# Kernel tuning notes

Measured on AMD Instinct MI355X. Metric: run time of the kernel, lower is better.

## Reference

```python
import jax, jax.numpy as jnp
import numpy as np

DIM = 1024
HEADS = 16
DIM_HEAD = 64


def setup_inputs() -> dict:
    key = jax.random.key(0)
    ks = jax.random.split(key, 6)
    b, n = 2, 2048
    x = jax.random.normal(ks[0], (b, n, DIM), dtype=jnp.float32)
    gamma = jnp.ones((DIM,), dtype=jnp.float32)
    w_qkv = jax.random.normal(ks[1], (DIM, 3 * HEADS * DIM_HEAD), dtype=jnp.float32) * (DIM ** -0.5)
    w_gates = jax.random.normal(ks[2], (DIM, HEADS), dtype=jnp.float32) * (DIM ** -0.5)
    b_gates = jnp.zeros((HEADS,), dtype=jnp.float32)
    w_out = jax.random.normal(ks[3], (HEADS * DIM_HEAD, DIM), dtype=jnp.float32) * ((HEADS * DIM_HEAD) ** -0.5)
    freqs = jax.random.uniform(ks[4], (DIM_HEAD // 2,), dtype=jnp.float32)
    return {"x": x, "gamma": gamma, "w_qkv": w_qkv, "w_gates": w_gates,
            "b_gates": b_gates, "w_out": w_out, "freqs": freqs}


def _rotate_half(t):
    # interleaved pairs: (x1, x2) -> (-x2, x1)
    tp = t.reshape(t.shape[:-1] + (t.shape[-1] // 2, 2))
    x1, x2 = tp[..., 0], tp[..., 1]
    return jnp.stack((-x2, x1), axis=-1).reshape(t.shape)


def reference(x, gamma, w_qkv, w_gates, b_gates, w_out, freqs):
    b, n, d = x.shape
    # RMSNorm variant: divide by L2 norm, scale by gamma * sqrt(dim)
    xn = x / jnp.linalg.norm(x, axis=-1, keepdims=True)
    xn = xn * gamma * (d ** 0.5)
    # QKV projection: (b, n, 3*H*D) -> q,k,v each (b, h, n, dh)
    qkv = xn @ w_qkv
    qkv = qkv.reshape(b, n, 3, HEADS, DIM_HEAD).transpose(2, 0, 3, 1, 4)
    q, k, v = qkv[0], qkv[1], qkv[2]
    # Inline RoPE (interleaved): freqs (n, dh)
    pos = jnp.arange(n, dtype=freqs.dtype)
    f = jnp.repeat(pos[:, None] * freqs[None, :], 2, axis=-1)  # (n, dh)
    cos_f, sin_f = jnp.cos(f), jnp.sin(f)
    q = q * cos_f + _rotate_half(q) * sin_f
    k = k * cos_f + _rotate_half(k) * sin_f
    # SDPA
    scale = DIM_HEAD ** -0.5
    scores = jnp.einsum('bhqd,bhkd->bhqk', q, k) * scale
    attn = jax.nn.softmax(scores, axis=-1)
    out = jnp.einsum('bhqk,bhkd->bhqd', attn, v)  # (b, h, n, dh)
    # per-head sigmoid gate from normalized input
    gates = xn @ w_gates + b_gates  # (b, n, h)
    out = out * jax.nn.sigmoid(gates.transpose(0, 2, 1))[..., None]
    # merge heads and output projection
    out = out.transpose(0, 2, 1, 3).reshape(b, n, HEADS * DIM_HEAD)
    return out @ w_out
```

## Files before the change

### kernel.cpp

```cpp
#include <hip/hip_runtime.h>

typedef __bf16 bf16_t;
typedef __bf16 bf16x8 __attribute__((ext_vector_type(8)));
typedef __bf16 bf16x4 __attribute__((ext_vector_type(4)));
typedef float f32x4 __attribute__((ext_vector_type(4)));

#define B_  2
#define N_  2048
#define D_  1024
#define H_  16
#define DH_ 64

#define QSCALE 0.18033688011112042f
#define NEGC  -11.541560327111707f

#if __has_builtin(__builtin_amdgcn_exp2f)
#define EXP2F(x) __builtin_amdgcn_exp2f(x)
#else
#define EXP2F(x) exp2f(x)
#endif

#define GLL16(g, l) __builtin_amdgcn_global_load_lds( \
    (const __attribute__((address_space(1))) void*)(g), \
    (__attribute__((address_space(3))) void*)(l), 16, 0, 0)

__device__ __forceinline__ int xcd_swizzle_id() {
  int id = blockIdx.y * gridDim.x + blockIdx.x;
  int cpx = (gridDim.x * gridDim.y) >> 3;
  return (id & 7) * cpx + (id >> 3);
}

__global__ __launch_bounds__(256) void k_trig(const float* __restrict__ freqs,
    float* __restrict__ tc, float* __restrict__ ts) {
  int idx = blockIdx.x * 256 + threadIdx.x;
  int n = idx >> 5, j = idx & 31;
  float f = (float)n * freqs[j];
  tc[idx] = cosf(f);
  ts[idx] = sinf(f);
}

__global__ __launch_bounds__(256) void k_rmsnorm_gates(const float* __restrict__ x,
    const float* __restrict__ gamma, const float* __restrict__ wg,
    const float* __restrict__ bg, bf16_t* __restrict__ xn, float* __restrict__ gsig) {
  int row = blockIdx.x;
  const float4* xr = (const float4*)(x + (size_t)row * D_);
  int tid = threadIdx.x;
  float4 v = xr[tid];
  float ss = v.x*v.x + v.y*v.y + v.z*v.z + v.w*v.w;
  #pragma unroll
  for (int off = 32; off > 0; off >>= 1) ss += __shfl_down(ss, off);
  __shared__ float red4[4];
  if ((tid & 63) == 0) red4[tid >> 6] = ss;
  __syncthreads();
  float scale = 32.0f * rsqrtf(red4[0] + red4[1] + red4[2] + red4[3]);
  float4 g = ((const float4*)gamma)[tid];
  bf16x4 o;
  o[0] = (bf16_t)(v.x * scale * g.x);
  o[1] = (bf16_t)(v.y * scale * g.y);
  o[2] = (bf16_t)(v.z * scale * g.z);
  o[3] = (bf16_t)(v.w * scale * g.w);
  *(bf16x4*)(xn + (size_t)row * D_ + tid * 4) = o;
  float xv[4] = {(float)o[0], (float)o[1], (float)o[2], (float)o[3]};
  float part[16];
  #pragma unroll
  for (int h = 0; h < 16; ++h) part[h] = 0.f;
  #pragma unroll
  for (int j = 0; j < 4; ++j) {
    const float4* wr = (const float4*)&wg[(size_t)(tid * 4 + j) * 16];
    #pragma unroll
    for (int q = 0; q < 4; ++q) {
      float4 w4 = wr[q];
      part[q * 4 + 0] += xv[j] * w4.x;
      part[q * 4 + 1] += xv[j] * w4.y;
      part[q * 4 + 2] += xv[j] * w4.z;
      part[q * 4 + 3] += xv[j] * w4.w;
    }
  }
  __shared__ float red[256][17];
  #pragma unroll
  for (int h = 0; h < 16; ++h) red[tid][h] = part[h];
  __syncthreads();
  int h = tid & 15, grp = tid >> 4;
  float s = 0.f;
  #pragma unroll
  for (int k = 0; k < 16; ++k) s += red[grp * 16 + k][h];
  __syncthreads();
  red[grp][h] = s;
  __syncthreads();
  if (tid < 16) {
    float acc = bg[tid];
    #pragma unroll
    for (int k = 0; k < 16; ++k) acc += red[k][tid];
    gsig[(size_t)row * 16 + tid] = 1.0f / (1.0f + __expf(-acc));
  }
}

__global__ __launch_bounds__(256) void k_transpose_cvt(const float* __restrict__ W,
    bf16_t* __restrict__ Wt, int R, int C) {
  __shared__ float tile[32][33];
  int c0 = blockIdx.x * 32, r0 = blockIdx.y * 32;
  int tx = threadIdx.x & 31, ty = threadIdx.x >> 5;
  #pragma unroll
  for (int i = 0; i < 4; ++i) {
    int r = ty + i * 8;
    tile[r][tx] = W[(size_t)(r0 + r) * C + c0 + tx];
  }
  __syncthreads();
  #pragma unroll
  for (int i = 0; i < 4; ++i) {
    int rr = ty + i * 8;
    Wt[(size_t)(c0 + rr) * R + r0 + tx] = (bf16_t)tile[tx][rr];
  }
}

__global__ __launch_bounds__(256) void k_gemm_qkv(const bf16_t* __restrict__ A,
    const bf16_t* __restrict__ Bt, const float* __restrict__ tc,
    const float* __restrict__ ts, bf16_t* __restrict__ Qb,
    bf16_t* __restrict__ Kb, bf16_t* __restrict__ Vb) {
  constexpr int BK = 32, K = 1024;
  constexpr int TP = 136;
  __shared__ __align__(16) bf16_t As[128 * BK];
  __shared__ __align__(16) bf16_t Bs[128 * BK];
  __shared__ __align__(16) bf16_t Tt[128 * TP];
  int tid = threadIdx.x, wave = tid >> 6, lane = tid & 63;
  int l16 = lane & 15, quad = lane >> 4;
  int id = blockIdx.y * 32 + blockIdx.x;
  int xcd = id & 7, local = id >> 3;
  int bxi = (xcd & 3) * 8 + (local & 7);
  int byi = (xcd >> 2) * 12 + (local >> 3);
  int bm = bxi * 128, bn = byi * 128;
  int wm = (wave >> 1) * 64, wn = (wave & 1) * 64;
  int srow = wave * 32 + (lane >> 2);
  int scol = (lane & 3) * 8;
  const bf16_t* gA0 = &A [(size_t)(bm + srow)      * K + scol];
  const bf16_t* gA1 = &A [(size_t)(bm + srow + 16) * K + scol];
  const bf16_t* gB0 = &Bt[(size_t)(bn + srow)      * K + scol];
  const bf16_t* gB1 = &Bt[(size_t)(bn + srow + 16) * K + scol];
  bf16_t* lA0 = &As[(wave * 32)      * BK];
  bf16_t* lA1 = &As[(wave * 32 + 16) * BK];
  bf16_t* lB0 = &Bs[(wave * 32)      * BK];
  bf16_t* lB1 = &Bs[(wave * 32 + 16) * BK];
  f32x4 acc[4][4] = {};
  for (int k0 = 0; k0 < K; k0 += BK) {
    GLL16(gA0 + k0, lA0);
    GLL16(gA1 + k0, lA1);
    GLL16(gB0 + k0, lB0);
    GLL16(gB1 + k0, lB1);
    __syncthreads();
    bf16x8 af[4], bfr[4];
    #pragma unroll
    for (int t = 0; t < 4; ++t) {
      af[t]  = *(const bf16x8*)&As[(wm + t * 16 + l16) * BK + quad * 8];
      bfr[t] = *(const bf16x8*)&Bs[(wn + t * 16 + l16) * BK + quad * 8];
    }
    #pragma unroll
    for (int mt = 0; mt < 4; ++mt)
      #pragma unroll
      for (int nt = 0; nt < 4; ++nt)
        acc[mt][nt] = __builtin_amdgcn_mfma_f32_16x16x32_bf16(af[mt], bfr[nt], acc[mt][nt], 0, 0, 0);
    __syncthreads();
  }
  if (byi < 16) {
    float qs = (byi < 8) ? QSCALE : 1.0f;
    bf16_t* dst = (byi < 8) ? Qb : Kb;
    #pragma unroll
    for (int mt = 0; mt < 4; ++mt)
      #pragma unroll
      for (int r = 0; r < 4; ++r) {
        int row_l = wm + mt * 16 + quad * 4 + r;
        int n = (bm + row_l) & 2047;
        const float* cr = tc + n * 32;
        const float* sr = ts + n * 32;
        #pragma unroll
        for (int nt = 0; nt < 4; ++nt) {
          int col_l = wn + nt * 16 + l16;
          int d = (bn + col_l) & 63, j = d >> 1;
          float val = acc[mt][nt][r];
          float p = __shfl_xor(val, 1);
          float c = cr[j], s = sr[j];
          float o = (d & 1) ? (val * c + p * s) : (val * c - p * s);
          Tt[row_l * TP + col_l] = (bf16_t)(o * qs);
        }
      }
    __syncthreads();
    #pragma unroll
    for (int it = 0; it < 8; ++it) {
      int idx = tid + 256 * it;
      int row_l = idx >> 4, ck = (idx & 15) * 8;
      bf16x8 v = *(const bf16x8*)&Tt[row_l * TP + ck];
      int grow = bm + row_l, b = grow >> 11, n = grow & 2047;
      int col = bn + ck, h = (col >> 6) & 15, d = col & 63;
      *(bf16x8*)&dst[((size_t)(b * H_ + h) * N_ + n) * DH_ + d] = v;
    }
  } else {
    #pragma unroll
    for (int mt = 0; mt < 4; ++mt)
      #pragma unroll
      for (int nt = 0; nt < 4; ++nt) {
        int col_l = wn + nt * 16 + l16;
        int row0 = wm + mt * 16 + quad * 4;
        #pragma unroll
        for (int r = 0; r < 4; ++r)
          Tt[col_l * TP + row0 + r] = (bf16_t)acc[mt][nt][r];
      }
    __syncthreads();
    int b = bm >> 11, nb = bm & 2047;
    #pragma unroll
    for (int it = 0; it < 8; ++it) {
      int idx = tid + 256 * it;
      int col_l = idx >> 4, ck = (idx & 15) * 8;
      bf16x8 v = *(const bf16x8*)&Tt[col_l * TP + ck];
      int vcol = bn + col_l - 2048, h = vcol >> 6, d = vcol & 63;
      *(bf16x8*)&Vb[((size_t)(b * H_ + h) * DH_ + d) * N_ + nb + ck] = v;
    }
  }
}

__global__ __launch_bounds__(256) void k_gemm_bt_n64(const bf16_t* __restrict__ A,
    const bf16_t* __restrict__ Bt, float* __restrict__ C, int M, int N, int K) {
  constexpr int BK = 32;
  __shared__ __align__(16) bf16_t As[128 * BK];
  __shared__ __align__(16) bf16_t Bs[64 * BK];
  int tid = threadIdx.x, wave = tid >> 6, lane = tid & 63;
  int l16 = lane & 15, quad = lane >> 4;
  int swz = xcd_swizzle_id();
  int bxi = swz % gridDim.x, byi = swz / gridDim.x;
  int bm = bxi * 128, bn = byi * 64;
  int wm = (wave >> 1) * 64, wn = (wave & 1) * 32;
  int srow = wave * 32 + (lane >> 2);
  int scol = (lane & 3) * 8;
  const bf16_t* gA0 = &A [(size_t)(bm + srow)      * K + scol];
  const bf16_t* gA1 = &A [(size_t)(bm + srow + 16) * K + scol];
  int srB = wave * 16 + (lane >> 2);
  const bf16_t* gB0 = &Bt[(size_t)(bn + srB) * K + scol];
  bf16_t* lA0 = &As[(wave * 32)      * BK];
  bf16_t* lA1 = &As[(wave * 32 + 16) * BK];
  bf16_t* lB0 = &Bs[(wave * 16)      * BK];
  f32x4 acc[4][2] = {};
  for (int k0 = 0; k0 < K; k0 += BK) {
    GLL16(gA0 + k0, lA0);
    GLL16(gA1 + k0, lA1);
    GLL16(gB0 + k0, lB0);
    __syncthreads();
    bf16x8 af[4], bfr[2];
    #pragma unroll
    for (int t = 0; t < 4; ++t)
      af[t]  = *(const bf16x8*)&As[(wm + t * 16 + l16) * BK + quad * 8];
    #pragma unroll
    for (int t = 0; t < 2; ++t)
      bfr[t] = *(const bf16x8*)&Bs[(wn + t * 16 + l16) * BK + quad * 8];
    #pragma unroll
    for (int mt = 0; mt < 4; ++mt)
      #pragma unroll
      for (int nt = 0; nt < 2; ++nt)
        acc[mt][nt] = __builtin_amdgcn_mfma_f32_16x16x32_bf16(af[mt], bfr[nt], acc[mt][nt], 0, 0, 0);
    __syncthreads();
  }
  #pragma unroll
  for (int mt = 0; mt < 4; ++mt)
    #pragma unroll
    for (int nt = 0; nt < 2; ++nt)
      #pragma unroll
      for (int r = 0; r < 4; ++r) {
        int row = bm + wm + mt * 16 + quad * 4 + r;
        int col = bn + wn + nt * 16 + l16;
        C[(size_t)row * N + col] = acc[mt][nt][r];
      }
}

__global__ __launch_bounds__(256) void k_flash(const bf16_t* __restrict__ Qb,
    const bf16_t* __restrict__ Kb, const bf16_t* __restrict__ Vb,
    const float* __restrict__ gsig, bf16_t* __restrict__ Ao) {
  __shared__ __align__(16) bf16_t Ks[2][64 * 72];
  __shared__ __align__(16) bf16_t Vt[2][64 * 72];
  __shared__ __align__(16) bf16_t Ps[4][32 * 72];
  int swz = xcd_swizzle_id();
  int qblk = swz & 15, bh = swz >> 4;
  int b = bh >> 4, h = bh & 15;
  int tid = threadIdx.x, wave = tid >> 6, lane = tid & 63;
  int l16 = lane & 15, quad = lane >> 4;
  int qw = qblk * 128 + wave * 32;
  const bf16_t* Qh = Qb + (size_t)bh * N_ * DH_;
  const bf16_t* Kh = Kb + (size_t)bh * N_ * DH_;
  const bf16_t* Vh = Vb + (size_t)bh * DH_ * N_;
  bf16_t* Pw = Ps[wave];
  bf16x8 qf[2][2];
  #pragma unroll
  for (int qt = 0; qt < 2; ++qt)
    #pragma unroll
    for (int hf = 0; hf < 2; ++hf)
      qf[qt][hf] = *(const bf16x8*)&Qh[(size_t)(qw + qt * 16 + l16) * DH_ + hf * 32 + quad * 8];
  bf16x8 onesf;
  #pragma unroll
  for (int i = 0; i < 8; ++i) onesf[i] = (bf16_t)1.0f;
  f32x4 accO[2][4] = {};
  f32x4 accL[2] = {};
  int sk = tid >> 3;
  int sc = (tid & 7) * 8;
  bf16x8 rk0 = *(const bf16x8*)&Kh[(size_t)sk * DH_ + sc];
  bf16x8 rk1 = *(const bf16x8*)&Kh[(size_t)(sk + 32) * DH_ + sc];
  bf16x8 rv0 = *(const bf16x8*)&Vh[(size_t)sk * N_ + sc];
  bf16x8 rv1 = *(const bf16x8*)&Vh[(size_t)(sk + 32) * N_ + sc];
  *(bf16x8*)&Ks[0][sk * 72 + sc]        = rk0;
  *(bf16x8*)&Ks[0][(sk + 32) * 72 + sc] = rk1;
  *(bf16x8*)&Vt[0][sk * 72 + sc]        = rv0;
  *(bf16x8*)&Vt[0][(sk + 32) * 72 + sc] = rv1;
  __syncthreads();
  const f32x4 zinit = {NEGC, NEGC, NEGC, NEGC};
  for (int k0 = 0; k0 < N_; k0 += 64) {
    int cur = (k0 >> 6) & 1;
    const bf16_t* Kc = Ks[cur];
    const bf16_t* Vc = Vt[cur];
    int kn = k0 + 64;
    if (kn < N_) {
      rk0 = *(const bf16x8*)&Kh[(size_t)(kn + sk) * DH_ + sc];
      rk1 = *(const bf16x8*)&Kh[(size_t)(kn + sk + 32) * DH_ + sc];
      rv0 = *(const bf16x8*)&Vh[(size_t)sk * N_ + kn + sc];
      rv1 = *(const bf16x8*)&Vh[(size_t)(sk + 32) * N_ + kn + sc];
    }
    f32x4 st[4][2];
    __builtin_amdgcn_s_setprio(1);
    #pragma unroll
    for (int kt = 0; kt < 4; ++kt) {
      bf16x8 kf0 = *(const bf16x8*)&Kc[(kt * 16 + l16) * 72 + quad * 8];
      bf16x8 kf1 = *(const bf16x8*)&Kc[(kt * 16 + l16) * 72 + 32 + quad * 8];
      #pragma unroll
      for (int qt = 0; qt < 2; ++qt) {
        f32x4 z = zinit;
        z = __builtin_amdgcn_mfma_f32_16x16x32_bf16(kf0, qf[qt][0], z, 0, 0, 0);
        z = __builtin_amdgcn_mfma_f32_16x16x32_bf16(kf1, qf[qt][1], z, 0, 0, 0);
        st[kt][qt] = z;
      }
    }
    __builtin_amdgcn_s_setprio(0);
    #pragma unroll
    for (int qt = 0; qt < 2; ++qt)
      #pragma unroll
      for (int kt = 0; kt < 4; ++kt) {
        bf16x4 pk;
        #pragma unroll
        for (int r = 0; r < 4; ++r)
          pk[r] = (bf16_t)EXP2F(st[kt][qt][r]);
        *(bf16x4*)&Pw[(qt * 16 + l16) * 72 + kt * 16 + quad * 4] = pk;
      }
    bf16x8 pf[2][2];
    #pragma unroll
    for (int qt = 0; qt < 2; ++qt)
      #pragma unroll
      for (int hf = 0; hf < 2; ++hf)
        pf[qt][hf] = *(const bf16x8*)&Pw[(qt * 16 + l16) * 72 + hf * 32 + quad * 8];
    __builtin_amdgcn_s_setprio(1);
    #pragma unroll
    for (int qt = 0; qt < 2; ++qt) {
      accL[qt] = __builtin_amdgcn_mfma_f32_16x16x32_bf16(pf[qt][0], onesf, accL[qt], 0, 0, 0);
      accL[qt] = __builtin_amdgcn_mfma_f32_16x16x32_bf16(pf[qt][1], onesf, accL[qt], 0, 0, 0);
    }
    #pragma unroll
    for (int dt = 0; dt < 4; ++dt)
      #pragma unroll
      for (int hf = 0; hf < 2; ++hf) {
        bf16x8 vf = *(const bf16x8*)&Vc[(dt * 16 + l16) * 72 + hf * 32 + quad * 8];
        #pragma unroll
        for (int qt = 0; qt < 2; ++qt)
          accO[qt][dt] = __builtin_amdgcn_mfma_f32_16x16x32_bf16(pf[qt][hf], vf, accO[qt][dt], 0, 0, 0);
      }
    __builtin_amdgcn_s_setprio(0);
    if (kn < N_) {
      int nb = cur ^ 1;
      *(bf16x8*)&Ks[nb][sk * 72 + sc]        = rk0;
      *(bf16x8*)&Ks[nb][(sk + 32) * 72 + sc] = rk1;
      *(bf16x8*)&Vt[nb][sk * 72 + sc]        = rv0;
      *(bf16x8*)&Vt[nb][(sk + 32) * 72 + sc] = rv1;
    }
    __syncthreads();
  }
  #pragma unroll
  for (int qt = 0; qt < 2; ++qt)
    #pragma unroll
    for (int r = 0; r < 4; ++r) {
      int q = qw + qt * 16 + quad * 4 + r;
      float g = gsig[((size_t)b * N_ + q) * H_ + h];
      float ginv = g / accL[qt][r];
      #pragma unroll
      for (int dt = 0; dt < 4; ++dt)
        Ao[((size_t)b * N_ + q) * (H_ * DH_) + h * DH_ + dt * 16 + l16] =
            (bf16_t)(accO[qt][dt][r] * ginv);
    }
}

extern "C" void kernel_launch(void* const* d_in, const int* in_sizes, int n_in,
                              void* d_out, int out_size, void* d_ws, size_t ws_size,
                              hipStream_t stream) {
  (void)in_sizes; (void)n_in; (void)out_size; (void)ws_size;
  const float* x      = (const float*)d_in[0];
  const float* gamma  = (const float*)d_in[1];
  const float* w_qkv  = (const float*)d_in[2];
  const float* w_gate = (const float*)d_in[3];
  const float* b_gate = (const float*)d_in[4];
  const float* w_out  = (const float*)d_in[5];
  const float* freqs  = (const float*)d_in[6];
  float* out = (float*)d_out;
  char* ws = (char*)d_ws;
  bf16_t* xn    = (bf16_t*)(ws);
  bf16_t* wqkvT = (bf16_t*)(ws + ((size_t)8  << 20));
  bf16_t* woutT = (bf16_t*)(ws + ((size_t)14 << 20));
  bf16_t* Qb    = (bf16_t*)(ws + ((size_t)16 << 20));
  bf16_t* Kb    = (bf16_t*)(ws + ((size_t)24 << 20));
  bf16_t* Vb    = (bf16_t*)(ws + ((size_t)32 << 20));
  float*  gsig  = (float*) (ws + ((size_t)40 << 20));
  bf16_t* attn  = (bf16_t*)(ws + ((size_t)41 << 20));
  float*  trigc = (float*) (ws + ((size_t)49 << 20));
  float*  trigs = (float*) (ws + ((size_t)50 << 20));

  k_trig<<<256, 256, 0, stream>>>(freqs, trigc, trigs);
  k_transpose_cvt<<<dim3(3072 / 32, 1024 / 32), 256, 0, stream>>>(w_qkv, wqkvT, 1024, 3072);
  k_transpose_cvt<<<dim3(1024 / 32, 1024 / 32), 256, 0, stream>>>(w_out, woutT, 1024, 1024);
  k_rmsnorm_gates<<<4096, 256, 0, stream>>>(x, gamma, w_gate, b_gate, xn, gsig);
  k_gemm_qkv<<<dim3(32, 24), 256, 0, stream>>>(xn, wqkvT, trigc, trigs, Qb, Kb, Vb);
  k_flash<<<dim3(16, 32), 256, 0, stream>>>(Qb, Kb, Vb, gsig, attn);
  k_gemm_bt_n64<<<dim3(32, 16), 256, 0, stream>>>(attn, woutT, out, 4096, 1024, 1024);
}
```

Measured before the change: 239.7 us.

## Fuse prep kernels into one launch and double-buffer QKV GEMM LDS tiles

The trig, weight-transpose and RMSNorm/gate kernels are merged into a single k_prep launch that picks its role from the block index. This cuts three launches and lets the small jobs share the GPU at once. The QKV GEMM now double-buffers its A/B LDS tiles inside one shared buffer, which is reused by the epilogue transpose tile. It prefetches the next K-slice with global_load_lds while computing on the current one. This hides global-load latency but depends on the end-of-loop barrier for correctness.

```diff
diff --git a/kernel.cpp b/kernel.cpp
--- a/kernel.cpp
+++ b/kernel.cpp
@@ -30,86 +30,92 @@
   return (id & 7) * cpx + (id >> 3);
 }
 
-__global__ __launch_bounds__(256) void k_trig(const float* __restrict__ freqs,
-    float* __restrict__ tc, float* __restrict__ ts) {
-  int idx = blockIdx.x * 256 + threadIdx.x;
-  int n = idx >> 5, j = idx & 31;
-  float f = (float)n * freqs[j];
-  tc[idx] = cosf(f);
-  ts[idx] = sinf(f);
-}
-
-__global__ __launch_bounds__(256) void k_rmsnorm_gates(const float* __restrict__ x,
-    const float* __restrict__ gamma, const float* __restrict__ wg,
-    const float* __restrict__ bg, bf16_t* __restrict__ xn, float* __restrict__ gsig) {
-  int row = blockIdx.x;
-  const float4* xr = (const float4*)(x + (size_t)row * D_);
-  int tid = threadIdx.x;
-  float4 v = xr[tid];
-  float ss = v.x*v.x + v.y*v.y + v.z*v.z + v.w*v.w;
-  #pragma unroll
-  for (int off = 32; off > 0; off >>= 1) ss += __shfl_down(ss, off);
-  __shared__ float red4[4];
-  if ((tid & 63) == 0) red4[tid >> 6] = ss;
-  __syncthreads();
-  float scale = 32.0f * rsqrtf(red4[0] + red4[1] + red4[2] + red4[3]);
-  float4 g = ((const float4*)gamma)[tid];
-  bf16x4 o;
-  o[0] = (bf16_t)(v.x * scale * g.x);
-  o[1] = (bf16_t)(v.y * scale * g.y);
-  o[2] = (bf16_t)(v.z * scale * g.z);
-  o[3] = (bf16_t)(v.w * scale * g.w);
-  *(bf16x4*)(xn + (size_t)row * D_ + tid * 4) = o;
-  float xv[4] = {(float)o[0], (float)o[1], (float)o[2], (float)o[3]};
-  float part[16];
-  #pragma unroll
-  for (int h = 0; h < 16; ++h) part[h] = 0.f;
-  #pragma unroll
-  for (int j = 0; j < 4; ++j) {
-    const float4* wr = (const float4*)&wg[(size_t)(tid * 4 + j) * 16];
-    #pragma unroll
-    for (int q = 0; q < 4; ++q) {
-      float4 w4 = wr[q];
-      part[q * 4 + 0] += xv[j] * w4.x;
-      part[q * 4 + 1] += xv[j] * w4.y;
-      part[q * 4 + 2] += xv[j] * w4.z;
-      part[q * 4 + 3] += xv[j] * w4.w;
-    }
-  }
-  __shared__ float red[256][17];
-  #pragma unroll
-  for (int h = 0; h < 16; ++h) red[tid][h] = part[h];
-  __syncthreads();
-  int h = tid & 15, grp = tid >> 4;
-  float s = 0.f;
-  #pragma unroll
-  for (int k = 0; k < 16; ++k) s += red[grp * 16 + k][h];
-  __syncthreads();
-  red[grp][h] = s;
-  __syncthreads();
-  if (tid < 16) {
-    float acc = bg[tid];
-    #pragma unroll
-    for (int k = 0; k < 16; ++k) acc += red[k][tid];
-    gsig[(size_t)row * 16 + tid] = 1.0f / (1.0f + __expf(-acc));
-  }
-}
-
-__global__ __launch_bounds__(256) void k_transpose_cvt(const float* __restrict__ W,
-    bf16_t* __restrict__ Wt, int R, int C) {
-  __shared__ float tile[32][33];
-  int c0 = blockIdx.x * 32, r0 = blockIdx.y * 32;
-  int tx = threadIdx.x & 31, ty = threadIdx.x >> 5;
-  #pragma unroll
-  for (int i = 0; i < 4; ++i) {
-    int r = ty + i * 8;
-    tile[r][tx] = W[(size_t)(r0 + r) * C + c0 + tx];
-  }
-  __syncthreads();
-  #pragma unroll
-  for (int i = 0; i < 4; ++i) {
-    int rr = ty + i * 8;
-    Wt[(size_t)(c0 + rr) * R + r0 + tx] = (bf16_t)tile[tx][rr];
+__global__ __launch_bounds__(256) void k_prep(
+    const float* __restrict__ x, const float* __restrict__ gamma,
+    const float* __restrict__ wg, const float* __restrict__ bg,
+    bf16_t* __restrict__ xn, float* __restrict__ gsig,
+    const float* __restrict__ w_qkv, bf16_t* __restrict__ wqkvT,
+    const float* __restrict__ w_out, bf16_t* __restrict__ woutT,
+    const float* __restrict__ freqs, float* __restrict__ tc, float* __restrict__ ts) {
+  __shared__ __align__(16) char smem_raw[17424];
+  int id = blockIdx.x, tid = threadIdx.x;
+  if (id < 4096) {
+    float* red4 = (float*)smem_raw;
+    float (*red)[17] = (float(*)[17])(smem_raw + 16);
+    int row = id;
+    const float4* xr = (const float4*)(x + (size_t)row * D_);
+    float4 v = xr[tid];
+    float ss = v.x*v.x + v.y*v.y + v.z*v.z + v.w*v.w;
+    #pragma unroll
+    for (int off = 32; off > 0; off >>= 1) ss += __shfl_down(ss, off);
+    if ((tid & 63) == 0) red4[tid >> 6] = ss;
+    __syncthreads();
+    float scale = 32.0f * rsqrtf(red4[0] + red4[1] + red4[2] + red4[3]);
+    float4 g = ((const float4*)gamma)[tid];
+    bf16x4 o;
+    o[0] = (bf16_t)(v.x * scale * g.x);
+    o[1] = (bf16_t)(v.y * scale * g.y);
+    o[2] = (bf16_t)(v.z * scale * g.z);
+    o[3] = (bf16_t)(v.w * scale * g.w);
+    *(bf16x4*)(xn + (size_t)row * D_ + tid * 4) = o;
+    float xv[4] = {(float)o[0], (float)o[1], (float)o[2], (float)o[3]};
+    float part[16];
+    #pragma unroll
+    for (int h = 0; h < 16; ++h) part[h] = 0.f;
+    #pragma unroll
+    for (int j = 0; j < 4; ++j) {
+      const float4* wr = (const float4*)&wg[(size_t)(tid * 4 + j) * 16];
+      #pragma unroll
+      for (int q = 0; q < 4; ++q) {
+        float4 w4 = wr[q];
+        part[q * 4 + 0] += xv[j] * w4.x;
+        part[q * 4 + 1] += xv[j] * w4.y;
+        part[q * 4 + 2] += xv[j] * w4.z;
+        part[q * 4 + 3] += xv[j] * w4.w;
+      }
+    }
+    #pragma unroll
+    for (int h = 0; h < 16; ++h) red[tid][h] = part[h];
+    __syncthreads();
+    int h = tid & 15, grp = tid >> 4;
+    float s = 0.f;
+    #pragma unroll
+    for (int k = 0; k < 16; ++k) s += red[grp * 16 + k][h];
+    __syncthreads();
+    red[grp][h] = s;
+    __syncthreads();
+    if (tid < 16) {
+      float acc = bg[tid];
+      #pragma unroll
+      for (int k = 0; k < 16; ++k) acc += red[k][tid];
+      gsig[(size_t)row * 16 + tid] = 1.0f / (1.0f + __expf(-acc));
+    }
+  } else if (id < 8192) {
+    const float* W; bf16_t* Wt; int R, C, bx, by;
+    if (id < 7168) { int local = id - 4096; W = w_qkv; Wt = wqkvT; R = 1024; C = 3072;
+                     bx = local % 96; by = local / 96; }
+    else           { int local = id - 7168; W = w_out; Wt = woutT; R = 1024; C = 1024;
+                     bx = local & 31; by = local >> 5; }
+    float (*tile)[33] = (float(*)[33])smem_raw;
+    int c0 = bx * 32, r0 = by * 32;
+    int tx = tid & 31, ty = tid >> 5;
+    #pragma unroll
+    for (int i = 0; i < 4; ++i) {
+      int r = ty + i * 8;
+      tile[r][tx] = W[(size_t)(r0 + r) * C + c0 + tx];
+    }
+    __syncthreads();
+    #pragma unroll
+    for (int i = 0; i < 4; ++i) {
+      int rr = ty + i * 8;
+      Wt[(size_t)(c0 + rr) * R + r0 + tx] = (bf16_t)tile[tx][rr];
+    }
+  } else {
+    int idx = (id - 8192) * 256 + tid;
+    int n = idx >> 5, j = idx & 31;
+    float f = (float)n * freqs[j];
+    tc[idx] = cosf(f);
+    ts[idx] = sinf(f);
   }
 }
 
@@ -119,9 +125,10 @@
     bf16_t* __restrict__ Kb, bf16_t* __restrict__ Vb) {
   constexpr int BK = 32, K = 1024;
   constexpr int TP = 136;
-  __shared__ __align__(16) bf16_t As[128 * BK];
-  __shared__ __align__(16) bf16_t Bs[128 * BK];
-  __shared__ __align__(16) bf16_t Tt[128 * TP];
+  __shared__ __align__(16) char smem[128 * TP * 2];
+  bf16_t* As0 = (bf16_t*)smem;
+  bf16_t* Bs0 = (bf16_t*)(smem + 16384);
+  bf16_t* Tt  = (bf16_t*)smem;
   int tid = threadIdx.x, wave = tid >> 6, lane = tid & 63;
   int l16 = lane & 15, quad = lane >> 4;
   int id = blockIdx.y * 32 + blockIdx.x;
@@ -136,22 +143,30 @@
   const bf16_t* gA1 = &A [(size_t)(bm + srow + 16) * K + scol];
   const bf16_t* gB0 = &Bt[(size_t)(bn + srow)      * K + scol];
   const bf16_t* gB1 = &Bt[(size_t)(bn + srow + 16) * K + scol];
-  bf16_t* lA0 = &As[(wave * 32)      * BK];
-  bf16_t* lA1 = &As[(wave * 32 + 16) * BK];
-  bf16_t* lB0 = &Bs[(wave * 32)      * BK];
-  bf16_t* lB1 = &Bs[(wave * 32 + 16) * BK];
+  bf16_t* lA0 = &As0[(wave * 32)      * BK];
+  bf16_t* lA1 = &As0[(wave * 32 + 16) * BK];
+  bf16_t* lB0 = &Bs0[(wave * 32)      * BK];
+  bf16_t* lB1 = &Bs0[(wave * 32 + 16) * BK];
   f32x4 acc[4][4] = {};
+  GLL16(gA0, lA0); GLL16(gA1, lA1); GLL16(gB0, lB0); GLL16(gB1, lB1);
+  __syncthreads();
   for (int k0 = 0; k0 < K; k0 += BK) {
-    GLL16(gA0 + k0, lA0);
-    GLL16(gA1 + k0, lA1);
-    GLL16(gB0 + k0, lB0);
-    GLL16(gB1 + k0, lB1);
-    __syncthreads();
+    int cur = (k0 >> 5) & 1;
+    int co  = cur * 4096;
+    int nxt = 4096 - co;
+    if (k0 + BK < K) {
+      GLL16(gA0 + k0 + BK, lA0 + nxt);
+      GLL16(gA1 + k0 + BK, lA1 + nxt);
+      GLL16(gB0 + k0 + BK, lB0 + nxt);
+      GLL16(gB1 + k0 + BK, lB1 + nxt);
+    }
+    const bf16_t* Asc = As0 + co;
+    const bf16_t* Bsc = Bs0 + co;
     bf16x8 af[4], bfr[4];
     #pragma unroll
     for (int t = 0; t < 4; ++t) {
-      af[t]  = *(const bf16x8*)&As[(wm + t * 16 + l16) * BK + quad * 8];
-      bfr[t] = *(const bf16x8*)&Bs[(wn + t * 16 + l16) * BK + quad * 8];
+      af[t]  = *(const bf16x8*)&Asc[(wm + t * 16 + l16) * BK + quad * 8];
+      bfr[t] = *(const bf16x8*)&Bsc[(wn + t * 16 + l16) * BK + quad * 8];
     }
     #pragma unroll
     for (int mt = 0; mt < 4; ++mt)
@@ -412,10 +427,8 @@
   float*  trigc = (float*) (ws + ((size_t)49 << 20));
   float*  trigs = (float*) (ws + ((size_t)50 << 20));
 
-  k_trig<<<256, 256, 0, stream>>>(freqs, trigc, trigs);
-  k_transpose_cvt<<<dim3(3072 / 32, 1024 / 32), 256, 0, stream>>>(w_qkv, wqkvT, 1024, 3072);
-  k_transpose_cvt<<<dim3(1024 / 32, 1024 / 32), 256, 0, stream>>>(w_out, woutT, 1024, 1024);
-  k_rmsnorm_gates<<<4096, 256, 0, stream>>>(x, gamma, w_gate, b_gate, xn, gsig);
+  k_prep<<<8448, 256, 0, stream>>>(x, gamma, w_gate, b_gate, xn, gsig,
+                                   w_qkv, wqkvT, w_out, woutT, freqs, trigc, trigs);
   k_gemm_qkv<<<dim3(32, 24), 256, 0, stream>>>(xn, wqkvT, trigc, trigs, Qb, Kb, Vb);
   k_flash<<<dim3(16, 32), 256, 0, stream>>>(Qb, Kb, Vb, gsig, attn);
   k_gemm_bt_n64<<<dim3(32, 16), 256, 0, stream>>>(attn, woutT, out, 4096, 1024, 1024);
```

Result: faster. 224.9 us (-6.2%).
